# Optimization experiments

Hardware: AMD Instinct MI355X
Metric: run time of the kernel (lower is better)

Reference implementation:

```python
import jax, jax.numpy as jnp
import numpy as np

STRIDE = 14
C_LOCAL = 2
NUM_HEADS = 12


def sparse_attention_mask(n_tokens, stride_length=STRIDE, c=C_LOCAL, mode='fixed'):
    q = jnp.arange(n_tokens)[:, None]  # row index Q
    k = jnp.arange(n_tokens)[None, :]  # col index K
    if mode == 'fixed':
        m1 = (q // stride_length) == (k // stride_length)
        m2 = ((k % stride_length) >= stride_length - c) & ((k % stride_length) <= stride_length)
        return m1 | m2
    elif mode == 'strided':
        m1 = jnp.abs(q - k) <= stride_length
        m2 = ((q - k) % stride_length) == 0
        return m1 | m2


def setup_inputs() -> dict:
    key = jax.random.key(0)
    ks = jax.random.split(key, 5)
    B, N, C = 16, 1024, 768
    return {
        'x': jax.random.normal(ks[0], (B, N, C), dtype=jnp.float32),
        'w_qkv': jax.random.normal(ks[1], (3 * C, C), dtype=jnp.float32) * (1.0 / np.sqrt(C)),
        'b_qkv': jax.random.normal(ks[2], (3 * C,), dtype=jnp.float32) * 0.02,
        'w_proj': jax.random.normal(ks[3], (C, C), dtype=jnp.float32) * (1.0 / np.sqrt(C)),
        'b_proj': jax.random.normal(ks[4], (C,), dtype=jnp.float32) * 0.02,
    }


def reference(x, w_qkv, b_qkv, w_proj, b_proj):
    B, N, C = x.shape
    H = NUM_HEADS
    D = C // H
    mask = sparse_attention_mask(N, mode='fixed')  # [N, N] bool

    # qkv projection: [B,N,3C] -> [3,B,H,N,D]
    qkv = x @ w_qkv.T + b_qkv
    qkv = qkv.reshape(B, N, 3, H, D).transpose(2, 0, 3, 1, 4)
    q, k, v = qkv[0], qkv[1], qkv[2]

    # SDPA with default scale = 1/sqrt(head_dim) and boolean attn_mask
    scale = 1.0 / jnp.sqrt(jnp.asarray(D, dtype=x.dtype))
    scores = jnp.einsum('bhnd,bhmd->bhnm', q, k) * scale
    scores = jnp.where(mask[None, None, :, :], scores, jnp.finfo(scores.dtype).min)
    attn = jax.nn.softmax(scores, axis=-1)
    out = jnp.einsum('bhnm,bhmd->bhnd', attn, v)

    # merge heads and output projection
    out = out.transpose(0, 2, 1, 3).reshape(B, N, C)
    return out @ w_proj.T + b_proj
```

## Files before the change

### kernel.cpp

```cpp
#include <hip/hip_runtime.h>
#include <stdint.h>

typedef unsigned short u16;
typedef __attribute__((ext_vector_type(8))) short bf16x8;
typedef __attribute__((ext_vector_type(4))) short s16x4;
typedef __attribute__((ext_vector_type(4))) float f32x4;

__device__ __forceinline__ u16 f2bf(float f) {
  uint32_t x = __builtin_bit_cast(uint32_t, f);
  uint32_t r = (x + 0x7fffu + ((x >> 16) & 1u)) >> 16;
  return (u16)r;
}
__device__ __forceinline__ float bf2f(u16 u) {
  return __builtin_bit_cast(float, (uint32_t)u << 16);
}

typedef __attribute__((address_space(3))) uint32_t lds_u32;
typedef const __attribute__((address_space(1))) uint32_t glb_u32;
__device__ __forceinline__ void gload_lds16(const void* g, void* l) {
  __builtin_amdgcn_global_load_lds(
      reinterpret_cast<glb_u32*>(reinterpret_cast<uintptr_t>(g)),
      reinterpret_cast<lds_u32*>(reinterpret_cast<uintptr_t>(l)),
      16, 0, 0);
}

__global__ void cvt_split_kernel(const float* __restrict__ in, u16* __restrict__ hi,
                                 u16* __restrict__ lo, int n4) {
  typedef __attribute__((ext_vector_type(4))) float float4v;
  int i = blockIdx.x * 256 + threadIdx.x;
  const int stride = gridDim.x * 256;
  for (; i < n4; i += stride) {
    float4v v = *(const float4v*)(in + (size_t)i * 4);
    s16x4 hv;
#pragma unroll
    for (int j = 0; j < 4; ++j) hv[j] = (short)f2bf(v[j]);
    *(s16x4*)(hi + (size_t)i * 4) = hv;
    if (lo) {
      s16x4 lv;
#pragma unroll
      for (int j = 0; j < 4; ++j) lv[j] = (short)f2bf(v[j] - bf2f((u16)hv[j]));
      *(s16x4*)(lo + (size_t)i * 4) = lv;
    }
  }
}

template <int OUTF32>
__global__ __launch_bounds__(256, 2) void gemm_bt(
    const u16* __restrict__ A, const u16* __restrict__ B0,
    const float* __restrict__ bias, float* __restrict__ outF, u16* __restrict__ outB,
    int Ndim, int Kdim) {
  __shared__ u16 sA[2][128 * 32];
  __shared__ u16 sB[2][128 * 32];

  const int tid = threadIdx.x;
  const int lane = tid & 63;
  const int wr = (tid >> 6) >> 1;
  const int wc = (tid >> 6) & 1;
  const int brow = blockIdx.x * 128;
  const int bcol = blockIdx.y * 128;

  auto stage = [&](int buf, int k0) {
#pragma unroll
    for (int j = 0; j < 2; ++j) {
      const int c = j * 256 + tid;
      const int r = c >> 2;
      const int off = (c & 3) * 8;
      gload_lds16(A + (size_t)(brow + r) * Kdim + k0 + off, &sA[buf][c * 8]);
      gload_lds16(B0 + (size_t)(bcol + r) * Kdim + k0 + off, &sB[buf][c * 8]);
    }
  };

  f32x4 acc[4][4] = {};

  stage(0, 0);
  __syncthreads();

  const int nt = Kdim >> 5;
  for (int t = 0; t < nt; ++t) {
    const int cur = t & 1;
    if (t + 1 < nt) stage(cur ^ 1, (t + 1) << 5);

    bf16x8 a[4], b[4];
#pragma unroll
    for (int m = 0; m < 4; ++m)
      a[m] = *(const bf16x8*)&sA[cur][(wr * 64 + m * 16 + (lane & 15)) * 32 + (lane >> 4) * 8];
#pragma unroll
    for (int n = 0; n < 4; ++n)
      b[n] = *(const bf16x8*)&sB[cur][(wc * 64 + n * 16 + (lane & 15)) * 32 + (lane >> 4) * 8];
#pragma unroll
    for (int m = 0; m < 4; ++m)
#pragma unroll
      for (int n = 0; n < 4; ++n)
        acc[m][n] = __builtin_amdgcn_mfma_f32_16x16x32_bf16(a[m], b[n], acc[m][n], 0, 0, 0);

    __syncthreads();
  }

  const int r0 = (lane >> 4) * 4;
  const int cn = lane & 15;
#pragma unroll
  for (int n = 0; n < 4; ++n) {
    const int colg = bcol + wc * 64 + n * 16 + cn;
    const float bv = bias[colg];
#pragma unroll
    for (int m = 0; m < 4; ++m) {
      const int rowg = brow + wr * 64 + m * 16 + r0;
#pragma unroll
      for (int r = 0; r < 4; ++r) {
        const float v = acc[m][n][r] + bv;
        if (OUTF32)
          outF[(size_t)(rowg + r) * Ndim + colg] = v;
        else
          outB[(size_t)(rowg + r) * Ndim + colg] = f2bf(v);
      }
    }
  }
}

__global__ __launch_bounds__(256) void transpose_v_kernel(const u16* __restrict__ qkv,
                                                          u16* __restrict__ vt) {
  __shared__ u16 t[64][72];
  const int tid = threadIdx.x;
  const int nt = blockIdx.x, h = blockIdx.y, b = blockIdx.z;
  const u16* src = qkv + (size_t)(b * 1024 + nt * 64) * 2304 + 1536 + h * 64;
#pragma unroll
  for (int j = 0; j < 2; ++j) {
    const int c = j * 256 + tid;
    const int row = c >> 3;
    const int off = (c & 7) * 8;
    *(bf16x8*)&t[row][off] = *(const bf16x8*)(src + (size_t)row * 2304 + off);
  }
  __syncthreads();
  u16* dst = vt + (size_t)(b * 12 + h) * 64 * 1024 + nt * 64;
#pragma unroll
  for (int j = 0; j < 2; ++j) {
    const int c = j * 256 + tid;
    const int drow = c >> 3;
    const int noff = (c & 7) * 8;
    bf16x8 o;
#pragma unroll
    for (int i = 0; i < 8; ++i) o[i] = (short)t[noff + i][drow];
    *(bf16x8*)(dst + (size_t)drow * 1024 + noff) = o;
  }
}

__global__ __launch_bounds__(256) void gather_global_kernel(const u16* __restrict__ qkv,
                                                            u16* __restrict__ kgc,
                                                            u16* __restrict__ vgc) {
  __shared__ u16 tl[192][72];
  const int tid = threadIdx.x;
  const int h = blockIdx.x % 12;
  const int b = blockIdx.x / 12;
  const u16* Kg = qkv + (size_t)(b * 1024) * 2304 + 768 + h * 64;
  const u16* Vg = qkv + (size_t)(b * 1024) * 2304 + 1536 + h * 64;
  u16* kout = kgc + (size_t)blockIdx.x * 192 * 64;
  u16* vout = vgc + (size_t)blockIdx.x * 64 * 192;

  for (int t = tid; t < 1536; t += 256) {
    const int s = t >> 3, ch = t & 7;
    bf16x8 kv = {}, vv = {};
    if (s < 146) {
      const int tok = (s >> 1) * 14 + 12 + (s & 1);
      kv = *(const bf16x8*)(Kg + (size_t)tok * 2304 + ch * 8);
      vv = *(const bf16x8*)(Vg + (size_t)tok * 2304 + ch * 8);
    }
    *(bf16x8*)(kout + s * 64 + ch * 8) = kv;
    *(bf16x8*)&tl[s][ch * 8] = vv;
  }
  __syncthreads();
  for (int t = tid; t < 64 * 24; t += 256) {
    const int d = t / 24, c8 = (t % 24) * 8;
    bf16x8 o;
#pragma unroll
    for (int i = 0; i < 8; ++i) o[i] = (short)tl[c8 + i][d];
    *(bf16x8*)(vout + (size_t)d * 192 + c8) = o;
  }
}

__global__ __launch_bounds__(256, 2) void attn_kernel(const u16* __restrict__ qkv,
                                                      const u16* __restrict__ vt,
                                                      const u16* __restrict__ kgc,
                                                      const u16* __restrict__ vgc,
                                                      u16* __restrict__ ao) {
  __shared__ u16 sQ[64 * 64];
  __shared__ u16 sK[2][64 * 64];
  __shared__ u16 sV[2][64 * 64];
  __shared__ u16 sP[4][16 * 72];

  const int tid = threadIdx.x;
  const int lane = tid & 63;
  const int wid = tid >> 6;
  const int qt = blockIdx.x, h = blockIdx.y, b = blockIdx.z;
  const int q0 = qt * 64;
  const int colL = lane & 15;
  const int kgrp = lane >> 4;
  const int bh = b * 12 + h;

  const u16* Qg = qkv + (size_t)(b * 1024 + q0) * 2304 + h * 64;
  const u16* Kg = qkv + (size_t)(b * 1024) * 2304 + 768 + h * 64;
  const u16* Vt = vt + (size_t)bh * 64 * 1024;
  const u16* Kc = kgc + (size_t)bh * 192 * 64;
  const u16* Vc = vgc + (size_t)bh * 64 * 192;

  const int first_blk = q0 / 14;
  const int tok0a = (first_blk * 14) & ~7;

  auto stage_kv = [&](int buf, int it) {
    if (it < 3) {
#pragma unroll
      for (int j = 0; j < 2; ++j) {
        const int c = j * 256 + tid;
        const int row = c >> 3;
        const int sb = ((c & 7) * 16) ^ ((row & 7) << 4);
        gload_lds16((const char*)(Kc + (size_t)(it * 64 + row) * 64) + sb, &sK[buf][c * 8]);
        gload_lds16((const char*)(Vc + (size_t)row * 192 + it * 64) + sb, &sV[buf][c * 8]);
      }
    } else {
      const int tc0 = tok0a + (it - 3) * 64;
#pragma unroll
      for (int j = 0; j < 2; ++j) {
        const int c = j * 256 + tid;
        const int row = c >> 3;
        const int sb = ((c & 7) * 16) ^ ((row & 7) << 4);
        const int ktok = min(tc0 + row, 1023);
        gload_lds16((const char*)(Kg + (size_t)ktok * 2304) + sb, &sK[buf][c * 8]);
        const int vb = min(tc0 * 2 + sb, 2032);
        gload_lds16((const char*)(Vt + (size_t)row * 1024) + vb, &sV[buf][c * 8]);
      }
    }
  };

#pragma unroll
  for (int j = 0; j < 2; ++j) {
    const int c = j * 256 + tid;
    const int row = c >> 3;
    const int off = (c & 7) * 8;
    gload_lds16(Qg + (size_t)row * 2304 + off, &sQ[c * 8]);
  }
  stage_kv(0, 0);
  __syncthreads();

  bf16x8 qf[2];
#pragma unroll
  for (int ks = 0; ks < 2; ++ks)
    qf[ks] = *(const bf16x8*)&sQ[(wid * 16 + colL) * 64 + ks * 32 + kgrp * 8];

  int qblk[4];
#pragma unroll
  for (int r = 0; r < 4; ++r) qblk[r] = (q0 + wid * 16 + kgrp * 4 + r) / 14;

  const float SCL = 0.125f * 1.44269504088896f;
  const float NEG = -3e38f;
  float mrun[4] = {NEG, NEG, NEG, NEG};
  float lsum[4] = {0.f, 0.f, 0.f, 0.f};
  f32x4 oacc[4] = {};

  for (int it = 0; it < 5; ++it) {
    const int cur = it & 1;
    if (it + 1 < 5) stage_kv(cur ^ 1, it + 1);

    f32x4 s[4] = {};
#pragma unroll
    for (int n = 0; n < 4; ++n) {
      const int row = n * 16 + colL;
#pragma unroll
      for (int ks = 0; ks < 2; ++ks) {
        const int cb = (ks * 32 + kgrp * 8) * 2;
        bf16x8 kf = *(const bf16x8*)((const char*)&sK[cur][0] + row * 128 + (cb ^ ((row & 7) << 4)));
        s[n] = __builtin_amdgcn_mfma_f32_16x16x32_bf16(qf[ks], kf, s[n], 0, 0, 0);
      }
    }

    float sv[4][4];
    if (it < 3) {
#pragma unroll
      for (int n = 0; n < 4; ++n) {
        const bool gv = (it * 64 + n * 16 + colL) < 146;
#pragma unroll
        for (int r = 0; r < 4; ++r) sv[n][r] = gv ? s[n][r] * SCL : NEG;
      }
    } else {
      const int tc0 = tok0a + (it - 3) * 64;
#pragma unroll
      for (int n = 0; n < 4; ++n) {
        const int t = tc0 + n * 16 + colL;
        const int tb = t / 14;
        const bool cv = (t < 1024) && ((t - tb * 14) < 12);
#pragma unroll
        for (int r = 0; r < 4; ++r) {
          const bool ok = cv && (tb == qblk[r]);
          sv[n][r] = ok ? s[n][r] * SCL : NEG;
        }
      }
    }

    float pmax[4];
#pragma unroll
    for (int r = 0; r < 4; ++r) {
      float v = fmaxf(fmaxf(sv[0][r], sv[1][r]), fmaxf(sv[2][r], sv[3][r]));
#pragma unroll
      for (int msk = 1; msk <= 8; msk <<= 1) v = fmaxf(v, __shfl_xor(v, msk));
      pmax[r] = v;
    }

    float corr[4], psum[4];
#pragma unroll
    for (int r = 0; r < 4; ++r) {
      const float mn = fmaxf(mrun[r], pmax[r]);
      corr[r] = exp2f(mrun[r] - mn);
      mrun[r] = mn;
      psum[r] = 0.f;
    }

    float p[4][4];
#pragma unroll
    for (int n = 0; n < 4; ++n)
#pragma unroll
      for (int r = 0; r < 4; ++r) {
        p[n][r] = exp2f(sv[n][r] - mrun[r]);
        psum[r] += p[n][r];
      }

#pragma unroll
    for (int r = 0; r < 4; ++r) {
      float v = psum[r];
#pragma unroll
      for (int msk = 1; msk <= 8; msk <<= 1) v += __shfl_xor(v, msk);
      lsum[r] = lsum[r] * corr[r] + v;
    }

#pragma unroll
    for (int n = 0; n < 4; ++n)
#pragma unroll
      for (int r = 0; r < 4; ++r)
        sP[wid][(kgrp * 4 + r) * 72 + n * 16 + colL] = f2bf(p[n][r]);

#pragma unroll
    for (int dn = 0; dn < 4; ++dn)
#pragma unroll
      for (int r = 0; r < 4; ++r) oacc[dn][r] *= corr[r];

#pragma unroll
    for (int ks = 0; ks < 2; ++ks) {
      bf16x8 pf = *(const bf16x8*)&sP[wid][colL * 72 + ks * 32 + kgrp * 8];
#pragma unroll
      for (int dn = 0; dn < 4; ++dn) {
        const int vrow = dn * 16 + colL;
        const int cb = (ks * 32 + kgrp * 8) * 2;
        bf16x8 vf = *(const bf16x8*)((const char*)&sV[cur][0] + vrow * 128 + (cb ^ ((vrow & 7) << 4)));
        oacc[dn] = __builtin_amdgcn_mfma_f32_16x16x32_bf16(pf, vf, oacc[dn], 0, 0, 0);
      }
    }

    __syncthreads();
  }

  float inv[4];
#pragma unroll
  for (int r = 0; r < 4; ++r) inv[r] = 1.0f / lsum[r];
#pragma unroll
  for (int dn = 0; dn < 4; ++dn)
#pragma unroll
    for (int r = 0; r < 4; ++r) {
      const int rowg = b * 1024 + q0 + wid * 16 + kgrp * 4 + r;
      const int colg = h * 64 + dn * 16 + colL;
      ao[(size_t)rowg * 768 + colg] = f2bf(oacc[dn][r] * inv[r]);
    }
}

extern "C" void kernel_launch(void* const* d_in, const int* in_sizes, int n_in,
                              void* d_out, int out_size, void* d_ws, size_t ws_size,
                              hipStream_t stream) {
  const float* x = (const float*)d_in[0];
  const float* w_qkv = (const float*)d_in[1];
  const float* b_qkv = (const float*)d_in[2];
  const float* w_proj = (const float*)d_in[3];
  const float* b_proj = (const float*)d_in[4];
  float* out = (float*)d_out;

  char* ws = (char*)d_ws;
  size_t off = 0;
  auto alloc = [&](size_t bytes) {
    char* p = ws + off;
    off += (bytes + 255) & ~(size_t)255;
    return p;
  };
  u16* x_bf = (u16*)alloc(16384ull * 768 * 2);
  u16* wq_bf = (u16*)alloc(2304ull * 768 * 2);
  u16* wp_bf = (u16*)alloc(768ull * 768 * 2);
  u16* qkvb = (u16*)alloc(16384ull * 2304 * 2);
  u16* vt = (u16*)alloc(192ull * 64 * 1024 * 2);
  u16* kgc = (u16*)alloc(192ull * 192 * 64 * 2);
  u16* vgc = (u16*)alloc(192ull * 64 * 192 * 2);
  u16* ao = x_bf;

  cvt_split_kernel<<<dim3(4096), dim3(256), 0, stream>>>(x, x_bf, nullptr, 16384 * 768 / 4);
  cvt_split_kernel<<<dim3(1728), dim3(256), 0, stream>>>(w_qkv, wq_bf, nullptr, 2304 * 768 / 4);
  cvt_split_kernel<<<dim3(576), dim3(256), 0, stream>>>(w_proj, wp_bf, nullptr, 768 * 768 / 4);

  gemm_bt<0><<<dim3(128, 18), dim3(256), 0, stream>>>(x_bf, wq_bf, b_qkv,
                                                      nullptr, qkvb, 2304, 768);
  transpose_v_kernel<<<dim3(16, 12, 16), dim3(256), 0, stream>>>(qkvb, vt);
  gather_global_kernel<<<dim3(192), dim3(256), 0, stream>>>(qkvb, kgc, vgc);
  attn_kernel<<<dim3(16, 12, 16), dim3(256), 0, stream>>>(qkvb, vt, kgc, vgc, ao);
  gemm_bt<1><<<dim3(128, 6), dim3(256), 0, stream>>>(ao, wp_bf, b_proj,
                                                     out, nullptr, 768, 768);
}
```

Before: 200.6 us.

## Enlarge GEMM tiles to 256x256 with triple-buffered swizzled LDS pipeline

Replaces the 128x128 bf16 GEMM with a 256x256-tile, 512-thread variant. Each wave now computes a 128x64 sub-tile with an 8x4 MFMA accumulator grid. Global-to-LDS loads become a three-stage pipeline using explicit vmcnt waits, with an XOR swizzle on LDS rows to cut bank conflicts and setprio around the MFMA block. The goal is more operand reuse and better overlap of load latency, at the cost of more registers and LDS per block. It also leaves far fewer blocks per GEMM (576 and 192), which may underfill the GPU.

New measurement: 221.8 us. 1.11x slower.

```diff
diff --git a/kernel.cpp b/kernel.cpp
--- a/kernel.cpp
+++ b/kernel.cpp
@@ -23,6 +23,8 @@
       reinterpret_cast<lds_u32*>(reinterpret_cast<uintptr_t>(l)),
       16, 0, 0);
 }
+
+__device__ __forceinline__ int swz(int r) { return (r & 3) ^ ((r >> 2) & 3); }
 
 __global__ void cvt_split_kernel(const float* __restrict__ in, u16* __restrict__ hi,
                                  u16* __restrict__ lo, int n4) {
@@ -45,66 +47,96 @@
 }
 
 template <int OUTF32>
-__global__ __launch_bounds__(256, 2) void gemm_bt(
+__global__ __launch_bounds__(512, 2) void gemm_bt2(
     const u16* __restrict__ A, const u16* __restrict__ B0,
     const float* __restrict__ bias, float* __restrict__ outF, u16* __restrict__ outB,
     int Ndim, int Kdim) {
-  __shared__ u16 sA[2][128 * 32];
-  __shared__ u16 sB[2][128 * 32];
+  __shared__ u16 sA[3][256 * 32];
+  __shared__ u16 sB[3][256 * 32];
 
   const int tid = threadIdx.x;
   const int lane = tid & 63;
-  const int wr = (tid >> 6) >> 1;
-  const int wc = (tid >> 6) & 1;
-  const int brow = blockIdx.x * 128;
-  const int bcol = blockIdx.y * 128;
-
-  auto stage = [&](int buf, int k0) {
+  const int wid = tid >> 6;
+  const int wr = wid >> 2;
+  const int wc = wid & 3;
+  const int brow = blockIdx.x * 256;
+  const int bcol = blockIdx.y * 256;
+  const int colL = lane & 15;
+  const int kgrp = lane >> 4;
+  const int NT = Kdim >> 5;
+
+  int srcA[2], srcB[2], ldsU[2];
+#pragma unroll
+  for (int j = 0; j < 2; ++j) {
+    const int u = (wid * 2 + j) * 64 + lane;
+    const int r = u >> 2;
+    const int sl = (u & 3) ^ swz(r);
+    srcA[j] = (brow + r) * Kdim + sl * 8;
+    srcB[j] = (bcol + r) * Kdim + sl * 8;
+    ldsU[j] = u * 8;
+  }
+
+  int oa[8], ob[4];
+#pragma unroll
+  for (int m = 0; m < 8; ++m) {
+    const int r = wr * 128 + m * 16 + colL;
+    oa[m] = r * 32 + ((kgrp ^ swz(r)) * 8);
+  }
+#pragma unroll
+  for (int n = 0; n < 4; ++n) {
+    const int r = wc * 64 + n * 16 + colL;
+    ob[n] = r * 32 + ((kgrp ^ swz(r)) * 8);
+  }
+
+  auto stage = [&](int buf, int t) {
+    const int k0 = t << 5;
 #pragma unroll
     for (int j = 0; j < 2; ++j) {
-      const int c = j * 256 + tid;
-      const int r = c >> 2;
-      const int off = (c & 3) * 8;
-      gload_lds16(A + (size_t)(brow + r) * Kdim + k0 + off, &sA[buf][c * 8]);
-      gload_lds16(B0 + (size_t)(bcol + r) * Kdim + k0 + off, &sB[buf][c * 8]);
+      gload_lds16(A + (size_t)(srcA[j] + k0), &sA[buf][ldsU[j]]);
+      gload_lds16(B0 + (size_t)(srcB[j] + k0), &sB[buf][ldsU[j]]);
     }
   };
 
-  f32x4 acc[4][4] = {};
+  f32x4 acc[8][4] = {};
 
   stage(0, 0);
-  __syncthreads();
-
-  const int nt = Kdim >> 5;
-  for (int t = 0; t < nt; ++t) {
-    const int cur = t & 1;
-    if (t + 1 < nt) stage(cur ^ 1, (t + 1) << 5);
-
-    bf16x8 a[4], b[4];
-#pragma unroll
-    for (int m = 0; m < 4; ++m)
-      a[m] = *(const bf16x8*)&sA[cur][(wr * 64 + m * 16 + (lane & 15)) * 32 + (lane >> 4) * 8];
-#pragma unroll
-    for (int n = 0; n < 4; ++n)
-      b[n] = *(const bf16x8*)&sB[cur][(wc * 64 + n * 16 + (lane & 15)) * 32 + (lane >> 4) * 8];
-#pragma unroll
-    for (int m = 0; m < 4; ++m)
+  stage(1, 1);
+  asm volatile("s_waitcnt vmcnt(4)" ::: "memory");
+  __builtin_amdgcn_s_barrier();
+
+  for (int t = 0; t < NT; ++t) {
+    const int cur = t % 3;
+    if (t + 2 < NT) stage((t + 2) % 3, t + 2);
+
+    bf16x8 a[8], b[4];
+#pragma unroll
+    for (int m = 0; m < 8; ++m) a[m] = *(const bf16x8*)&sA[cur][oa[m]];
+#pragma unroll
+    for (int n = 0; n < 4; ++n) b[n] = *(const bf16x8*)&sB[cur][ob[n]];
+
+    __builtin_amdgcn_s_setprio(1);
+#pragma unroll
+    for (int m = 0; m < 8; ++m)
 #pragma unroll
       for (int n = 0; n < 4; ++n)
         acc[m][n] = __builtin_amdgcn_mfma_f32_16x16x32_bf16(a[m], b[n], acc[m][n], 0, 0, 0);
-
-    __syncthreads();
-  }
-
-  const int r0 = (lane >> 4) * 4;
-  const int cn = lane & 15;
+    __builtin_amdgcn_s_setprio(0);
+
+    if (t + 2 < NT)
+      asm volatile("s_waitcnt vmcnt(4)" ::: "memory");
+    else
+      asm volatile("s_waitcnt vmcnt(0)" ::: "memory");
+    __builtin_amdgcn_s_barrier();
+  }
+
+  const int r0 = kgrp * 4;
 #pragma unroll
   for (int n = 0; n < 4; ++n) {
-    const int colg = bcol + wc * 64 + n * 16 + cn;
+    const int colg = bcol + wc * 64 + n * 16 + colL;
     const float bv = bias[colg];
 #pragma unroll
-    for (int m = 0; m < 4; ++m) {
-      const int rowg = brow + wr * 64 + m * 16 + r0;
+    for (int m = 0; m < 8; ++m) {
+      const int rowg = brow + wr * 128 + m * 16 + r0;
 #pragma unroll
       for (int r = 0; r < 4; ++r) {
         const float v = acc[m][n][r] + bv;
@@ -398,11 +430,11 @@
   cvt_split_kernel<<<dim3(1728), dim3(256), 0, stream>>>(w_qkv, wq_bf, nullptr, 2304 * 768 / 4);
   cvt_split_kernel<<<dim3(576), dim3(256), 0, stream>>>(w_proj, wp_bf, nullptr, 768 * 768 / 4);
 
-  gemm_bt<0><<<dim3(128, 18), dim3(256), 0, stream>>>(x_bf, wq_bf, b_qkv,
-                                                      nullptr, qkvb, 2304, 768);
+  gemm_bt2<0><<<dim3(64, 9), dim3(512), 0, stream>>>(x_bf, wq_bf, b_qkv,
+                                                     nullptr, qkvb, 2304, 768);
   transpose_v_kernel<<<dim3(16, 12, 16), dim3(256), 0, stream>>>(qkvb, vt);
   gather_global_kernel<<<dim3(192), dim3(256), 0, stream>>>(qkvb, kgc, vgc);
   attn_kernel<<<dim3(16, 12, 16), dim3(256), 0, stream>>>(qkvb, vt, kgc, vgc, ao);
-  gemm_bt<1><<<dim3(128, 6), dim3(256), 0, stream>>>(ao, wp_bf, b_proj,
+  gemm_bt2<1><<<dim3(64, 3), dim3(512), 0, stream>>>(ao, wp_bf, b_proj,
                                                      out, nullptr, 768, 768);
 }
```
